# Optimization experiments

Hardware: AMD Instinct MI355X
Metric: run time of the kernel (lower is better)

Reference implementation:

```python
import jax, jax.numpy as jnp
import numpy as np
from jax import lax

N, T, I, H, O = 2048, 512, 32, 64, 1

def setup_inputs() -> dict:
    key = jax.random.key(0)
    ks = jax.random.split(key, 7)
    s_ih = 1.0 / np.sqrt(H)
    return {
        "x": jax.random.normal(ks[0], (N, T, I), dtype=jnp.float32),
        "W_ih": jax.random.uniform(ks[1], (H, I), jnp.float32, -s_ih, s_ih),
        "W_hh": jax.random.uniform(ks[2], (H, H), jnp.float32, -s_ih, s_ih),
        "b_ih": jax.random.uniform(ks[3], (H,), jnp.float32, -s_ih, s_ih),
        "b_hh": jax.random.uniform(ks[4], (H,), jnp.float32, -s_ih, s_ih),
        "fc_w": jax.random.uniform(ks[5], (O, H), jnp.float32, -s_ih, s_ih),
        "fc_b": jax.random.uniform(ks[6], (O,), jnp.float32, -s_ih, s_ih),
    }

def reference(x, W_ih, W_hh, b_ih, b_hh, fc_w, fc_b):
    # Batched equivalent of the per-sample python loop: each sample starts
    # from the same hidden state of ones (self.hidden = torch.ones(...)).
    n, t = x.shape[0], x.shape[1]
    h0 = jnp.ones((n, W_hh.shape[0]), dtype=x.dtype)
    xs = jnp.swapaxes(x, 0, 1)  # [T, N, I] -> scan over time

    def step(h, xt):
        # Elman RNN with tanh (torch nn.RNN default nonlinearity)
        h_new = jnp.tanh(xt @ W_ih.T + b_ih + h @ W_hh.T + b_hh)
        return h_new, None

    hT, _ = lax.scan(step, h0, xs)  # hT: [N, H], last-timestep hidden = out[-1]
    return jax.nn.sigmoid(hT @ fc_w.T + fc_b)  # [N, O]
```

## Files before the change

kernel.cpp:

```cpp
#include <hip/hip_runtime.h>


#define RN 2048
#define RT 512
#define RI 32
#define RH 64

typedef _Float16 h4 __attribute__((ext_vector_type(4)));
typedef float    f4 __attribute__((ext_vector_type(4)));

__device__ __forceinline__ int pk2(float a, float b) {
    return __builtin_bit_cast(int, __builtin_amdgcn_cvt_pkrtz(a, b));
}
__device__ __forceinline__ h4 pack4(float a, float b, float c, float d) {
    union { h4 v; int i[2]; } u;
    u.i[0] = pk2(a, b);
    u.i[1] = pk2(c, d);
    return u.v;
}
__device__ __forceinline__ h4 packf4(f4 v) { return pack4(v[0], v[1], v[2], v[3]); }

__device__ __forceinline__ float tanh_fast(float z) {
    float e = __expf(2.0f * z);
    return 1.0f - __fdividef(2.0f, e + 1.0f);
}

__global__ __launch_bounds__(256, 1) void rnn_mfma4(
    const float* __restrict__ x,
    const float* __restrict__ W_ih,
    const float* __restrict__ W_hh,
    const float* __restrict__ b_ih,
    const float* __restrict__ b_hh,
    const float* __restrict__ fc_w,
    const float* __restrict__ fc_b,
    float* __restrict__ out)
{
    const int tid  = threadIdx.x;
    const int w    = tid >> 6;
    const int lane = tid & 63;
    const int col  = lane & 15;
    const int quad = lane >> 4;
    const int g    = blockIdx.x;

    __shared__ unsigned long long hb[2][4 * 64];
    __shared__ float ob[4][16];

    h4 Ahh[4];
#pragma unroll
    for (int kt = 0; kt < 4; ++kt) {
        f4 v = *(const f4*)(W_hh + (w * 16 + col) * RH + kt * 16 + quad * 4);
        Ahh[kt] = packf4(v);
    }
    h4 Aih[2];
#pragma unroll
    for (int kt = 0; kt < 2; ++kt) {
        f4 v = *(const f4*)(W_ih + (w * 16 + col) * RI + kt * 16 + quad * 4);
        Aih[kt] = packf4(v);
    }
    f4 biasv;
    {
        f4 bi = *(const f4*)(b_ih + w * 16 + quad * 4);
        f4 bh = *(const f4*)(b_hh + w * 16 + quad * 4);
        biasv = bi + bh;
    }

    const float* xb = x + (size_t)(g * 16 + col) * (RT * RI);
    f4 xbuf[4][2];
#pragma unroll
    for (int s = 0; s < 4; ++s) {
        xbuf[s][0] = *(const f4*)(xb + s * RI + quad * 4);
        xbuf[s][1] = *(const f4*)(xb + s * RI + 16 + quad * 4);
    }

    h4 Bh[4];
#pragma unroll
    for (int kt = 0; kt < 4; ++kt) Bh[kt] = pack4(1.f, 1.f, 1.f, 1.f);
    f4 hv;

    for (int t4 = 0; t4 < RT; t4 += 4) {
#pragma unroll
        for (int s = 0; s < 4; ++s) {
            const int t = t4 + s;
            h4 bx0 = packf4(xbuf[s][0]);
            h4 bx1 = packf4(xbuf[s][1]);
            int tn = t + 4; if (tn > RT - 1) tn = RT - 1;
            xbuf[s][0] = *(const f4*)(xb + tn * RI + quad * 4);
            xbuf[s][1] = *(const f4*)(xb + tn * RI + 16 + quad * 4);

            f4 c0 = __builtin_amdgcn_mfma_f32_16x16x16f16(Aih[0], bx0, biasv, 0, 0, 0);
            f4 c1 = __builtin_amdgcn_mfma_f32_16x16x16f16(Aih[1], bx1, f4{0.f, 0.f, 0.f, 0.f}, 0, 0, 0);
            c0 = __builtin_amdgcn_mfma_f32_16x16x16f16(Ahh[0], Bh[0], c0, 0, 0, 0);
            c1 = __builtin_amdgcn_mfma_f32_16x16x16f16(Ahh[1], Bh[1], c1, 0, 0, 0);
            c0 = __builtin_amdgcn_mfma_f32_16x16x16f16(Ahh[2], Bh[2], c0, 0, 0, 0);
            c1 = __builtin_amdgcn_mfma_f32_16x16x16f16(Ahh[3], Bh[3], c1, 0, 0, 0);
            f4 acc = c0 + c1;

            hv[0] = tanh_fast(acc[0]);
            hv[1] = tanh_fast(acc[1]);
            hv[2] = tanh_fast(acc[2]);
            hv[3] = tanh_fast(acc[3]);

            const int p = t & 1;
            hb[p][w * 64 + lane] = __builtin_bit_cast(unsigned long long, packf4(hv));
            __syncthreads();
            Bh[0] = __builtin_bit_cast(h4, hb[p][0 * 64 + lane]);
            Bh[1] = __builtin_bit_cast(h4, hb[p][1 * 64 + lane]);
            Bh[2] = __builtin_bit_cast(h4, hb[p][2 * 64 + lane]);
            Bh[3] = __builtin_bit_cast(h4, hb[p][3 * 64 + lane]);
        }
    }

    {
        f4 wv = *(const f4*)(fc_w + w * 16 + quad * 4);
        float s = wv[0] * hv[0] + wv[1] * hv[1] + wv[2] * hv[2] + wv[3] * hv[3];
        s += __shfl_xor(s, 16, 64);
        s += __shfl_xor(s, 32, 64);
        if (quad == 0) ob[w][col] = s;
        __syncthreads();
        if (w == 0 && lane < 16) {
            float logit = ob[0][lane] + ob[1][lane] + ob[2][lane] + ob[3][lane] + fc_b[0];
            out[g * 16 + lane] = __fdividef(1.0f, 1.0f + __expf(-logit));
        }
    }
}

extern "C" void kernel_launch(void* const* d_in, const int* in_sizes, int n_in,
                              void* d_out, int out_size, void* d_ws, size_t ws_size,
                              hipStream_t stream) {
    rnn_mfma4<<<RN / 16, 256, 0, stream>>>(
        (const float*)d_in[0], (const float*)d_in[1], (const float*)d_in[2],
        (const float*)d_in[3], (const float*)d_in[4], (const float*)d_in[5],
        (const float*)d_in[6], (float*)d_out);
}
```

Before: 308.7 us.

## Compute whole hidden state in one wavefront, removing LDS exchange and barriers

The recurrence for each 16-sample group moves from four wavefronts, each owning 16 hidden rows, to a single wavefront that holds all of W_hh and W_ih in registers and issues all 24 MFMAs per timestep. The new hidden state is packed straight into the B operands in registers. This removes the per-timestep LDS write/read and __syncthreads that the cross-wave hidden-state exchange needed. In exchange, one wave carries four times the serial MFMA and tanh work per step, uses more registers, and each CU runs only a quarter as many threads.

```diff
diff --git a/kernel.cpp b/kernel.cpp
--- a/kernel.cpp
+++ b/kernel.cpp
@@ -25,7 +25,7 @@
     return 1.0f - __fdividef(2.0f, e + 1.0f);
 }
 
-__global__ __launch_bounds__(256, 1) void rnn_mfma4(
+__global__ __launch_bounds__(64, 1) void rnn_mfma1(
     const float* __restrict__ x,
     const float* __restrict__ W_ih,
     const float* __restrict__ W_hh,
@@ -35,33 +35,35 @@
     const float* __restrict__ fc_b,
     float* __restrict__ out)
 {
-    const int tid  = threadIdx.x;
-    const int w    = tid >> 6;
-    const int lane = tid & 63;
+    const int lane = threadIdx.x & 63;
     const int col  = lane & 15;
     const int quad = lane >> 4;
     const int g    = blockIdx.x;
 
-    __shared__ unsigned long long hb[2][4 * 64];
-    __shared__ float ob[4][16];
+    h4 Ahh[4][4];
+#pragma unroll
+    for (int mt = 0; mt < 4; ++mt)
+#pragma unroll
+        for (int kt = 0; kt < 4; ++kt) {
+            f4 v = *(const f4*)(W_hh + (mt * 16 + col) * RH + kt * 16 + quad * 4);
+            Ahh[mt][kt] = packf4(v);
+        }
 
-    h4 Ahh[4];
+    h4 Aih[4][2];
 #pragma unroll
-    for (int kt = 0; kt < 4; ++kt) {
-        f4 v = *(const f4*)(W_hh + (w * 16 + col) * RH + kt * 16 + quad * 4);
-        Ahh[kt] = packf4(v);
-    }
-    h4 Aih[2];
+    for (int mt = 0; mt < 4; ++mt)
 #pragma unroll
-    for (int kt = 0; kt < 2; ++kt) {
-        f4 v = *(const f4*)(W_ih + (w * 16 + col) * RI + kt * 16 + quad * 4);
-        Aih[kt] = packf4(v);
-    }
-    f4 biasv;
-    {
-        f4 bi = *(const f4*)(b_ih + w * 16 + quad * 4);
-        f4 bh = *(const f4*)(b_hh + w * 16 + quad * 4);
-        biasv = bi + bh;
+        for (int kt = 0; kt < 2; ++kt) {
+            f4 v = *(const f4*)(W_ih + (mt * 16 + col) * RI + kt * 16 + quad * 4);
+            Aih[mt][kt] = packf4(v);
+        }
+
+    f4 bias[4];
+#pragma unroll
+    for (int mt = 0; mt < 4; ++mt) {
+        f4 bi = *(const f4*)(b_ih + mt * 16 + quad * 4);
+        f4 bh = *(const f4*)(b_hh + mt * 16 + quad * 4);
+        bias[mt] = bi + bh;
     }
 
     const float* xb = x + (size_t)(g * 16 + col) * (RT * RI);
@@ -75,7 +77,7 @@
     h4 Bh[4];
 #pragma unroll
     for (int kt = 0; kt < 4; ++kt) Bh[kt] = pack4(1.f, 1.f, 1.f, 1.f);
-    f4 hv;
+    f4 hv[4];
 
     for (int t4 = 0; t4 < RT; t4 += 4) {
 #pragma unroll
@@ -87,39 +89,44 @@
             xbuf[s][0] = *(const f4*)(xb + tn * RI + quad * 4);
             xbuf[s][1] = *(const f4*)(xb + tn * RI + 16 + quad * 4);
 
-            f4 c0 = __builtin_amdgcn_mfma_f32_16x16x16f16(Aih[0], bx0, biasv, 0, 0, 0);
-            f4 c1 = __builtin_amdgcn_mfma_f32_16x16x16f16(Aih[1], bx1, f4{0.f, 0.f, 0.f, 0.f}, 0, 0, 0);
-            c0 = __builtin_amdgcn_mfma_f32_16x16x16f16(Ahh[0], Bh[0], c0, 0, 0, 0);
-            c1 = __builtin_amdgcn_mfma_f32_16x16x16f16(Ahh[1], Bh[1], c1, 0, 0, 0);
-            c0 = __builtin_amdgcn_mfma_f32_16x16x16f16(Ahh[2], Bh[2], c0, 0, 0, 0);
-            c1 = __builtin_amdgcn_mfma_f32_16x16x16f16(Ahh[3], Bh[3], c1, 0, 0, 0);
-            f4 acc = c0 + c1;
+            f4 c[4];
+#pragma unroll
+            for (int mt = 0; mt < 4; ++mt)
+                c[mt] = __builtin_amdgcn_mfma_f32_16x16x16f16(Aih[mt][0], bx0, bias[mt], 0, 0, 0);
+#pragma unroll
+            for (int mt = 0; mt < 4; ++mt)
+                c[mt] = __builtin_amdgcn_mfma_f32_16x16x16f16(Aih[mt][1], bx1, c[mt], 0, 0, 0);
 
-            hv[0] = tanh_fast(acc[0]);
-            hv[1] = tanh_fast(acc[1]);
-            hv[2] = tanh_fast(acc[2]);
-            hv[3] = tanh_fast(acc[3]);
+#pragma unroll
+            for (int kt = 0; kt < 4; ++kt)
+#pragma unroll
+                for (int mt = 0; mt < 4; ++mt)
+                    c[mt] = __builtin_amdgcn_mfma_f32_16x16x16f16(Ahh[mt][kt], Bh[kt], c[mt], 0, 0, 0);
 
-            const int p = t & 1;
-            hb[p][w * 64 + lane] = __builtin_bit_cast(unsigned long long, packf4(hv));
-            __syncthreads();
-            Bh[0] = __builtin_bit_cast(h4, hb[p][0 * 64 + lane]);
-            Bh[1] = __builtin_bit_cast(h4, hb[p][1 * 64 + lane]);
-            Bh[2] = __builtin_bit_cast(h4, hb[p][2 * 64 + lane]);
-            Bh[3] = __builtin_bit_cast(h4, hb[p][3 * 64 + lane]);
+#pragma unroll
+            for (int mt = 0; mt < 4; ++mt) {
+                hv[mt][0] = tanh_fast(c[mt][0]);
+                hv[mt][1] = tanh_fast(c[mt][1]);
+                hv[mt][2] = tanh_fast(c[mt][2]);
+                hv[mt][3] = tanh_fast(c[mt][3]);
+                Bh[mt] = packf4(hv[mt]);
+            }
         }
     }
 
     {
-        f4 wv = *(const f4*)(fc_w + w * 16 + quad * 4);
-        float s = wv[0] * hv[0] + wv[1] * hv[1] + wv[2] * hv[2] + wv[3] * hv[3];
+        float s = 0.f;
+#pragma unroll
+        for (int mt = 0; mt < 4; ++mt) {
+            f4 wv = *(const f4*)(fc_w + mt * 16 + quad * 4);
+            s += wv[0] * hv[mt][0] + wv[1] * hv[mt][1]
+               + wv[2] * hv[mt][2] + wv[3] * hv[mt][3];
+        }
         s += __shfl_xor(s, 16, 64);
         s += __shfl_xor(s, 32, 64);
-        if (quad == 0) ob[w][col] = s;
-        __syncthreads();
-        if (w == 0 && lane < 16) {
-            float logit = ob[0][lane] + ob[1][lane] + ob[2][lane] + ob[3][lane] + fc_b[0];
-            out[g * 16 + lane] = __fdividef(1.0f, 1.0f + __expf(-logit));
+        if (quad == 0) {
+            float logit = s + fc_b[0];
+            out[g * 16 + col] = __fdividef(1.0f, 1.0f + __expf(-logit));
         }
     }
 }
@@ -127,7 +134,7 @@
 extern "C" void kernel_launch(void* const* d_in, const int* in_sizes, int n_in,
                               void* d_out, int out_size, void* d_ws, size_t ws_size,
                               hipStream_t stream) {
-    rnn_mfma4<<<RN / 16, 256, 0, stream>>>(
+    rnn_mfma1<<<RN / 16, 64, 0, stream>>>(
         (const float*)d_in[0], (const float*)d_in[1], (const float*)d_in[2],
         (const float*)d_in[3], (const float*)d_in[4], (const float*)d_in[5],
         (const float*)d_in[6], (float*)d_out);
```

New measurement: 503.5 us. 63.1% more time.
